# Kernel tuning notes

Hardware: AMD Instinct MI355X
Metric: run time of the kernel (lower is better)

The kernel has to match this reference:

```python
import jax, jax.numpy as jnp
import numpy as np

N_NODES = 50000
N_EDGES = 1600000
IN_DIM = 1024
HID = 128
N_GRAPHS = 64


def setup_inputs() -> dict:
    key = jax.random.key(0)
    ks = jax.random.split(key, 8)
    x = jax.random.normal(ks[0], (N_NODES, IN_DIM), dtype=jnp.float32)
    edge_index = jax.random.randint(ks[1], (2, N_EDGES), 0, N_NODES, dtype=jnp.int32)
    batch = jnp.sort(jax.random.randint(ks[2], (N_NODES,), 0, N_GRAPHS, dtype=jnp.int32))
    # GATConv parameters (single head, concat irrelevant for 1 head)
    glorot = 1.0 / np.sqrt(IN_DIM)
    W = jax.random.uniform(ks[3], (IN_DIM, HID), minval=-glorot, maxval=glorot, dtype=jnp.float32)
    ga = 1.0 / np.sqrt(HID)
    att_src = jax.random.uniform(ks[4], (HID,), minval=-ga, maxval=ga, dtype=jnp.float32)
    att_dst = jax.random.uniform(ks[5], (HID,), minval=-ga, maxval=ga, dtype=jnp.float32)
    bias = jnp.zeros((HID,), dtype=jnp.float32)
    return {"x": x, "W": W, "att_src": att_src, "att_dst": att_dst, "bias": bias,
            "edge_index": edge_index, "batch": batch, "num_graphs": N_GRAPHS}


def reference(x, W, att_src, att_dst, bias, edge_index, batch, num_graphs):
    N = x.shape[0]
    h = x @ W                               # [N, HID]
    # add self-loops (GATConv default add_self_loops=True)
    loops = jnp.arange(N, dtype=edge_index.dtype)
    src = jnp.concatenate([edge_index[0], loops])   # [E+N]
    dst = jnp.concatenate([edge_index[1], loops])
    a_src = h @ att_src                     # [N]
    a_dst = h @ att_dst                     # [N]
    e = jax.nn.leaky_relu(a_src[src] + a_dst[dst], negative_slope=0.2)  # [E+N]
    # scatter-softmax over incoming edges of each destination node
    m = jax.ops.segment_max(e, dst, num_segments=N)
    p = jnp.exp(e - m[dst])
    denom = jax.ops.segment_sum(p, dst, num_segments=N)
    alpha = p / denom[dst]                  # [E+N]
    # attention-weighted aggregation
    out = jax.ops.segment_sum(alpha[:, None] * h[src], dst, num_segments=N)  # [N, HID]
    out = jax.nn.relu(out + bias)
    # global max pool over graphs in the batch
    return jax.ops.segment_max(out, batch, num_segments=num_graphs)          # [G, HID]
```

## Files before the change

### kernel.cpp

```cpp
#include <hip/hip_runtime.h>
#include <hip/hip_bf16.h>

#define N_NODES 50000
#define N_EDGES 1600000
#define IN_DIM 1024
#define HID 128
#define AGG_WAVES 6144

typedef __bf16 bf16x8 __attribute__((ext_vector_type(8)));
typedef float f32x4 __attribute__((ext_vector_type(4)));
typedef __bf16 bf16x4 __attribute__((ext_vector_type(4)));

__device__ __forceinline__ float2 bf2f(unsigned u) {
    return make_float2(__uint_as_float(u << 16), __uint_as_float(u & 0xffff0000u));
}
__device__ __forceinline__ float lrelu(float v) { return v > 0.f ? v : 0.2f * v; }

__global__ void init_kernel(int* __restrict__ deg, float* __restrict__ out, int out_n) {
    int i = blockIdx.x * 256 + threadIdx.x;
    if (i < N_NODES) deg[i] = 0;
    if (i < out_n) out[i] = 0.0f;
}

__global__ void wtrans_kernel(const float* __restrict__ W, __bf16* __restrict__ wt) {
    int i = blockIdx.x * 256 + threadIdx.x;
    int n = i >> 10, k = i & 1023;
    wt[i] = (__bf16)W[(size_t)k * HID + n];
}

__global__ __launch_bounds__(256) void gemm_kernel(const float* __restrict__ x,
                                                   const __bf16* __restrict__ wt,
                                                   __bf16* __restrict__ h2,
                                                   const float* __restrict__ att_s,
                                                   const float* __restrict__ att_d,
                                                   float* __restrict__ o_as,
                                                   float* __restrict__ o_ad) {
    __shared__ __bf16 xa[128][40];
    __shared__ __bf16 wb[128][40];
    const int t = threadIdx.x;
    const int m0 = blockIdx.x * 128;
    const int wid = t >> 6, lane = t & 63;
    const int lm = lane & 15, q8 = (lane >> 4) * 8;
    const int rw0 = wid * 32;

    f32x4 acc[2][8] = {};
    for (int k0 = 0; k0 < IN_DIM; k0 += 32) {
#pragma unroll
        for (int l = 0; l < 4; ++l) {
            int f = t + l * 256;
            int row = f >> 3, kq = f & 7;
            int gr = m0 + row;
            float4 v = make_float4(0.f, 0.f, 0.f, 0.f);
            if (gr < N_NODES)
                v = *(const float4*)(x + (size_t)gr * IN_DIM + k0 + kq * 4);
            bf16x4 b; b[0] = (__bf16)v.x; b[1] = (__bf16)v.y; b[2] = (__bf16)v.z; b[3] = (__bf16)v.w;
            *(bf16x4*)&xa[row][kq * 4] = b;
        }
#pragma unroll
        for (int l = 0; l < 4; ++l) {
            int f = t + l * 256;
            int n = f >> 3, c = f & 7;
            *(uint2*)&wb[n][c * 4] = *(const uint2*)(wt + (size_t)n * IN_DIM + k0 + c * 4);
        }
        __syncthreads();
        bf16x8 af0 = *(const bf16x8*)&xa[rw0 + lm][q8];
        bf16x8 af1 = *(const bf16x8*)&xa[rw0 + 16 + lm][q8];
#pragma unroll
        for (int ct = 0; ct < 8; ++ct) {
            bf16x8 bfr = *(const bf16x8*)&wb[ct * 16 + lm][q8];
            acc[0][ct] = __builtin_amdgcn_mfma_f32_16x16x32_bf16(af0, bfr, acc[0][ct], 0, 0, 0);
            acc[1][ct] = __builtin_amdgcn_mfma_f32_16x16x32_bf16(af1, bfr, acc[1][ct], 0, 0, 0);
        }
        __syncthreads();
    }
    const int quad = lane >> 4;
    float attsf[8], attdf[8];
#pragma unroll
    for (int ct = 0; ct < 8; ++ct) {
        attsf[ct] = att_s[ct * 16 + lm];
        attdf[ct] = att_d[ct * 16 + lm];
    }
#pragma unroll
    for (int rt = 0; rt < 2; ++rt) {
#pragma unroll
        for (int reg = 0; reg < 4; ++reg) {
            int row = m0 + rw0 + rt * 16 + quad * 4 + reg;
            float ps = 0.f, pd = 0.f;
#pragma unroll
            for (int ct = 0; ct < 8; ++ct) {
                float v = acc[rt][ct][reg];
                ps = fmaf(v, attsf[ct], ps);
                pd = fmaf(v, attdf[ct], pd);
            }
#pragma unroll
            for (int o = 8; o; o >>= 1) {
                ps += __shfl_xor(ps, o);
                pd += __shfl_xor(pd, o);
            }
            if (row < N_NODES) {
                if (lm == 0) { o_as[row] = ps; o_ad[row] = pd; }
#pragma unroll
                for (int ct = 0; ct < 8; ++ct)
                    h2[(size_t)row * HID + ct * 16 + lm] = (__bf16)acc[rt][ct][reg];
            }
        }
    }
}

__global__ void hist_kernel(const int* __restrict__ ei, int* __restrict__ deg) {
    int e = blockIdx.x * 256 + threadIdx.x;
    if (e < N_EDGES) atomicAdd(&deg[ei[N_EDGES + e]], 1);
}

__global__ void scan1_kernel(const int* __restrict__ deg, int* __restrict__ bsum) {
    int b = blockIdx.x, t = threadIdx.x;
    int base = b * 1024 + t * 4;
    int s = 0;
#pragma unroll
    for (int j = 0; j < 4; ++j) {
        int idx = base + j;
        if (idx < N_NODES) s += deg[idx];
    }
    for (int o = 32; o; o >>= 1) s += __shfl_xor(s, o);
    __shared__ int wsum[4];
    int lane = t & 63, w = t >> 6;
    if (lane == 0) wsum[w] = s;
    __syncthreads();
    if (t == 0) bsum[b] = wsum[0] + wsum[1] + wsum[2] + wsum[3];
}

__global__ void scan2_kernel(const int* __restrict__ bsum, int* __restrict__ boff,
                             int* __restrict__ rowstart, int nb) {
    if (threadIdx.x == 0 && blockIdx.x == 0) {
        int run = 0;
        for (int i = 0; i < nb; ++i) { boff[i] = run; run += bsum[i]; }
        rowstart[N_NODES] = run;
    }
}

__global__ void scan3_kernel(int* __restrict__ deg, const int* __restrict__ boff,
                             int* __restrict__ rowstart) {
    int b = blockIdx.x, t = threadIdx.x;
    int base = b * 1024 + t * 4;
    int v[4]; int s = 0;
#pragma unroll
    for (int j = 0; j < 4; ++j) {
        int idx = base + j;
        v[j] = (idx < N_NODES) ? deg[idx] : 0;
        s += v[j];
    }
    int lane = t & 63, w = t >> 6;
    int inc = s;
    for (int o = 1; o < 64; o <<= 1) {
        int u = __shfl_up(inc, o);
        if (lane >= o) inc += u;
    }
    __shared__ int wt[4];
    if (lane == 63) wt[w] = inc;
    __syncthreads();
    int woff = 0;
    for (int i = 0; i < w; ++i) woff += wt[i];
    int run = woff + inc - s + boff[b];
#pragma unroll
    for (int j = 0; j < 4; ++j) {
        int idx = base + j;
        if (idx < N_NODES) {
            rowstart[idx] = run;
            run += v[j];
            deg[idx] = 0;
        }
    }
}

__global__ void scatter_kernel(const int* __restrict__ ei, const int* __restrict__ rowstart,
                               int* __restrict__ cursor, uint2* __restrict__ csrp,
                               const float* __restrict__ a_src) {
    int e = blockIdx.x * 256 + threadIdx.x;
    if (e >= N_EDGES) return;
    int s = ei[e], d = ei[N_EDGES + e];
    int pos = atomicAdd(&cursor[d], 1);
    uint2 v; v.x = (unsigned)s; v.y = __float_as_uint(a_src[s]);
    csrp[rowstart[d] + pos] = v;
}

__global__ __launch_bounds__(256, 6) void aggregate_kernel(
    const unsigned* __restrict__ h2u, const float* __restrict__ a_src,
    const float* __restrict__ a_dst, const int* __restrict__ rowstart,
    const uint2* __restrict__ csrp, const float* __restrict__ bias,
    const int* __restrict__ batch, float* __restrict__ out) {
    const int wid = threadIdx.x >> 6, lane = threadIdx.x & 63;
    const int w = blockIdx.x * 4 + wid;
    const int q = N_NODES / AGG_WAVES;
    const int r = N_NODES - q * AGG_WAVES;
    int n0 = w * q + (w < r ? w : r);
    int n1 = n0 + q + (w < r ? 1 : 0);
    const float b0 = bias[2 * lane], b1 = bias[2 * lane + 1];

    int gcur = -1;
    float m0 = 0.f, m1 = 0.f;
    for (int n = n0; n < n1; ++n) {
        int rs = rowstart[n], re = rowstart[n + 1];
        float adn = a_dst[n];
        float pself = __expf(lrelu(a_src[n] + adn));
        float2 hv = bf2f(h2u[(size_t)n * 64 + lane]);
        float denom = pself;
        float2 acc = make_float2(pself * hv.x, pself * hv.y);
        for (int base = rs; base < re; base += 64) {
            int cnt = re - base; if (cnt > 64) cnt = 64;
            uint2 sp = make_uint2(0u, 0u);
            bool valid = (base + lane < re);
            if (valid) sp = csrp[base + lane];
            float pe = valid ? __expf(lrelu(__uint_as_float(sp.y) + adn)) : 0.f;
            float ds = pe;
            for (int o = 32; o; o >>= 1) ds += __shfl_xor(ds, o);
            denom += ds;
            for (int e = 0; e < cnt; e += 16) {
                unsigned uu[16]; float pp[16];
#pragma unroll
                for (int i = 0; i < 16; ++i) {
                    unsigned src = (unsigned)__shfl((int)sp.x, e + i);
                    pp[i] = __shfl(pe, e + i);
                    uu[i] = h2u[(size_t)src * 64 + lane];
                }
#pragma unroll
                for (int i = 0; i < 16; ++i) {
                    float2 g = bf2f(uu[i]);
                    acc.x = fmaf(pp[i], g.x, acc.x);
                    acc.y = fmaf(pp[i], g.y, acc.y);
                }
            }
        }
        float inv = 1.0f / denom;
        float o0 = fmaxf(acc.x * inv + b0, 0.0f);
        float o1 = fmaxf(acc.y * inv + b1, 0.0f);
        int g = batch[n];
        if (g != gcur) {
            if (gcur >= 0) {
                unsigned* outp = (unsigned*)(out + (size_t)gcur * HID);
                atomicMax(&outp[2 * lane], __float_as_uint(m0));
                atomicMax(&outp[2 * lane + 1], __float_as_uint(m1));
            }
            gcur = g; m0 = o0; m1 = o1;
        } else {
            m0 = fmaxf(m0, o0); m1 = fmaxf(m1, o1);
        }
    }
    if (gcur >= 0) {
        unsigned* outp = (unsigned*)(out + (size_t)gcur * HID);
        atomicMax(&outp[2 * lane], __float_as_uint(m0));
        atomicMax(&outp[2 * lane + 1], __float_as_uint(m1));
    }
}

extern "C" void kernel_launch(void* const* d_in, const int* in_sizes, int n_in,
                              void* d_out, int out_size, void* d_ws, size_t ws_size,
                              hipStream_t stream) {
    const float* x     = (const float*)d_in[0];
    const float* W     = (const float*)d_in[1];
    const float* att_s = (const float*)d_in[2];
    const float* att_d = (const float*)d_in[3];
    const float* bias  = (const float*)d_in[4];
    const int*   ei    = (const int*)d_in[5];
    const int*   batch = (const int*)d_in[6];
    float*       out   = (float*)d_out;

    char* ws = (char*)d_ws;
    size_t off = 0;
    auto alloc = [&](size_t bytes) -> void* {
        void* p = ws + off;
        off += (bytes + 255) & ~(size_t)255;
        return p;
    };
    const int NB = (N_NODES + 1023) / 1024;
    __bf16* h2       = (__bf16*)alloc((size_t)N_NODES * HID * 2);
    __bf16* wt       = (__bf16*)alloc((size_t)HID * IN_DIM * 2);
    float*  a_src    = (float*)alloc((size_t)N_NODES * 4);
    float*  a_dst    = (float*)alloc((size_t)N_NODES * 4);
    int*    deg      = (int*)alloc((size_t)N_NODES * 4);
    int*    rowstart = (int*)alloc((size_t)(N_NODES + 1) * 4);
    int*    bsum     = (int*)alloc((size_t)NB * 4);
    int*    boff     = (int*)alloc((size_t)NB * 4);
    uint2*  csrp     = (uint2*)alloc((size_t)N_EDGES * 8);
    (void)ws_size; (void)in_sizes; (void)n_in;

    int init_n = (N_NODES > out_size ? N_NODES : out_size);
    hipLaunchKernelGGL(init_kernel, dim3((init_n + 255) / 256), dim3(256), 0, stream,
                       deg, out, out_size);
    hipLaunchKernelGGL(wtrans_kernel, dim3((HID * IN_DIM) / 256), dim3(256), 0, stream,
                       W, wt);
    hipLaunchKernelGGL(gemm_kernel, dim3((N_NODES + 127) / 128), dim3(256), 0, stream,
                       x, wt, h2, att_s, att_d, a_src, a_dst);
    hipLaunchKernelGGL(hist_kernel, dim3((N_EDGES + 255) / 256), dim3(256), 0, stream,
                       ei, deg);
    hipLaunchKernelGGL(scan1_kernel, dim3(NB), dim3(256), 0, stream, deg, bsum);
    hipLaunchKernelGGL(scan2_kernel, dim3(1), dim3(64), 0, stream, bsum, boff, rowstart, NB);
    hipLaunchKernelGGL(scan3_kernel, dim3(NB), dim3(256), 0, stream, deg, boff, rowstart);
    hipLaunchKernelGGL(scatter_kernel, dim3((N_EDGES + 255) / 256), dim3(256), 0, stream,
                       ei, rowstart, deg, csrp, a_src);
    hipLaunchKernelGGL(aggregate_kernel, dim3(AGG_WAVES / 4), dim3(256), 0, stream,
                       (const unsigned*)h2, a_src, a_dst, rowstart, csrp, bias, batch, out);
}
```

Baseline: 570.8 us.

## Halve GEMM tile rows, prefetch next K-slice into registers, merge prep kernels

The GEMM block tile shrinks from 128 to 64 rows, which doubles the grid size. The global loads for the next K-slice are issued into registers before the MFMAs on the current slice, overlapping memory latency with compute. The init and weight-transpose kernels are merged into one launch. The cost is that each W tile is reloaded by twice as many blocks, and each iteration now has an extra barrier.

Measured after the change: 540.1 us. 1.06x faster.

```diff
diff --git a/kernel.cpp b/kernel.cpp
--- a/kernel.cpp
+++ b/kernel.cpp
@@ -16,16 +16,15 @@
 }
 __device__ __forceinline__ float lrelu(float v) { return v > 0.f ? v : 0.2f * v; }
 
-__global__ void init_kernel(int* __restrict__ deg, float* __restrict__ out, int out_n) {
+__global__ void prep_kernel(const float* __restrict__ W, __bf16* __restrict__ wt,
+                            int* __restrict__ deg, float* __restrict__ out, int out_n) {
     int i = blockIdx.x * 256 + threadIdx.x;
     if (i < N_NODES) deg[i] = 0;
     if (i < out_n) out[i] = 0.0f;
-}
-
-__global__ void wtrans_kernel(const float* __restrict__ W, __bf16* __restrict__ wt) {
-    int i = blockIdx.x * 256 + threadIdx.x;
-    int n = i >> 10, k = i & 1023;
-    wt[i] = (__bf16)W[(size_t)k * HID + n];
+    if (i < HID * IN_DIM) {
+        int n = i >> 10, k = i & 1023;
+        wt[i] = (__bf16)W[(size_t)k * HID + n];
+    }
 }
 
 __global__ __launch_bounds__(256) void gemm_kernel(const float* __restrict__ x,
@@ -35,43 +34,73 @@
                                                    const float* __restrict__ att_d,
                                                    float* __restrict__ o_as,
                                                    float* __restrict__ o_ad) {
-    __shared__ __bf16 xa[128][40];
+    __shared__ __bf16 xa[64][40];
     __shared__ __bf16 wb[128][40];
     const int t = threadIdx.x;
-    const int m0 = blockIdx.x * 128;
+    const int m0 = blockIdx.x * 64;
     const int wid = t >> 6, lane = t & 63;
     const int lm = lane & 15, q8 = (lane >> 4) * 8;
-    const int rw0 = wid * 32;
-
-    f32x4 acc[2][8] = {};
-    for (int k0 = 0; k0 < IN_DIM; k0 += 32) {
-#pragma unroll
-        for (int l = 0; l < 4; ++l) {
+    const int rw0 = wid * 16;
+
+    const int xrow = t >> 2, xkq = (t & 3);
+    const int wn = t >> 1, wc2 = (t & 1);
+
+    float4 xs_reg[2];
+    uint2  ws_reg[4];
+
+    auto stage_regs = [&](int k0) {
+#pragma unroll
+        for (int l = 0; l < 2; ++l) {
             int f = t + l * 256;
             int row = f >> 3, kq = f & 7;
             int gr = m0 + row;
             float4 v = make_float4(0.f, 0.f, 0.f, 0.f);
             if (gr < N_NODES)
                 v = *(const float4*)(x + (size_t)gr * IN_DIM + k0 + kq * 4);
-            bf16x4 b; b[0] = (__bf16)v.x; b[1] = (__bf16)v.y; b[2] = (__bf16)v.z; b[3] = (__bf16)v.w;
-            *(bf16x4*)&xa[row][kq * 4] = b;
+            xs_reg[l] = v;
         }
 #pragma unroll
         for (int l = 0; l < 4; ++l) {
             int f = t + l * 256;
             int n = f >> 3, c = f & 7;
-            *(uint2*)&wb[n][c * 4] = *(const uint2*)(wt + (size_t)n * IN_DIM + k0 + c * 4);
-        }
-        __syncthreads();
-        bf16x8 af0 = *(const bf16x8*)&xa[rw0 + lm][q8];
-        bf16x8 af1 = *(const bf16x8*)&xa[rw0 + 16 + lm][q8];
+            ws_reg[l] = *(const uint2*)(wt + (size_t)n * IN_DIM + k0 + c * 4);
+        }
+    };
+    auto regs_to_lds = [&]() {
+#pragma unroll
+        for (int l = 0; l < 2; ++l) {
+            int f = t + l * 256;
+            int row = f >> 3, kq = f & 7;
+            bf16x4 b;
+            b[0] = (__bf16)xs_reg[l].x; b[1] = (__bf16)xs_reg[l].y;
+            b[2] = (__bf16)xs_reg[l].z; b[3] = (__bf16)xs_reg[l].w;
+            *(bf16x4*)&xa[row][kq * 4] = b;
+        }
+#pragma unroll
+        for (int l = 0; l < 4; ++l) {
+            int f = t + l * 256;
+            int n = f >> 3, c = f & 7;
+            *(uint2*)&wb[n][c * 4] = ws_reg[l];
+        }
+    };
+
+    f32x4 acc[8] = {};
+    stage_regs(0);
+    regs_to_lds();
+    __syncthreads();
+    for (int it = 0; it < 32; ++it) {
+        if (it + 1 < 32) stage_regs((it + 1) * 32);
+        bf16x8 af = *(const bf16x8*)&xa[rw0 + lm][q8];
 #pragma unroll
         for (int ct = 0; ct < 8; ++ct) {
             bf16x8 bfr = *(const bf16x8*)&wb[ct * 16 + lm][q8];
-            acc[0][ct] = __builtin_amdgcn_mfma_f32_16x16x32_bf16(af0, bfr, acc[0][ct], 0, 0, 0);
-            acc[1][ct] = __builtin_amdgcn_mfma_f32_16x16x32_bf16(af1, bfr, acc[1][ct], 0, 0, 0);
-        }
-        __syncthreads();
+            acc[ct] = __builtin_amdgcn_mfma_f32_16x16x32_bf16(af, bfr, acc[ct], 0, 0, 0);
+        }
+        if (it + 1 < 32) {
+            __syncthreads();
+            regs_to_lds();
+            __syncthreads();
+        }
     }
     const int quad = lane >> 4;
     float attsf[8], attdf[8];
@@ -81,30 +110,28 @@
         attdf[ct] = att_d[ct * 16 + lm];
     }
 #pragma unroll
-    for (int rt = 0; rt < 2; ++rt) {
-#pragma unroll
-        for (int reg = 0; reg < 4; ++reg) {
-            int row = m0 + rw0 + rt * 16 + quad * 4 + reg;
-            float ps = 0.f, pd = 0.f;
-#pragma unroll
-            for (int ct = 0; ct < 8; ++ct) {
-                float v = acc[rt][ct][reg];
-                ps = fmaf(v, attsf[ct], ps);
-                pd = fmaf(v, attdf[ct], pd);
-            }
-#pragma unroll
-            for (int o = 8; o; o >>= 1) {
-                ps += __shfl_xor(ps, o);
-                pd += __shfl_xor(pd, o);
-            }
-            if (row < N_NODES) {
-                if (lm == 0) { o_as[row] = ps; o_ad[row] = pd; }
-#pragma unroll
-                for (int ct = 0; ct < 8; ++ct)
-                    h2[(size_t)row * HID + ct * 16 + lm] = (__bf16)acc[rt][ct][reg];
-            }
-        }
-    }
+    for (int reg = 0; reg < 4; ++reg) {
+        int row = m0 + rw0 + quad * 4 + reg;
+        float ps = 0.f, pd = 0.f;
+#pragma unroll
+        for (int ct = 0; ct < 8; ++ct) {
+            float v = acc[ct][reg];
+            ps = fmaf(v, attsf[ct], ps);
+            pd = fmaf(v, attdf[ct], pd);
+        }
+#pragma unroll
+        for (int o = 8; o; o >>= 1) {
+            ps += __shfl_xor(ps, o);
+            pd += __shfl_xor(pd, o);
+        }
+        if (row < N_NODES) {
+            if (lm == 0) { o_as[row] = ps; o_ad[row] = pd; }
+#pragma unroll
+            for (int ct = 0; ct < 8; ++ct)
+                h2[(size_t)row * HID + ct * 16 + lm] = (__bf16)acc[ct][reg];
+        }
+    }
+    (void)xrow; (void)xkq; (void)wn; (void)wc2;
 }
 
 __global__ void hist_kernel(const int* __restrict__ ei, int* __restrict__ deg) {
@@ -283,12 +310,9 @@
     uint2*  csrp     = (uint2*)alloc((size_t)N_EDGES * 8);
     (void)ws_size; (void)in_sizes; (void)n_in;
 
-    int init_n = (N_NODES > out_size ? N_NODES : out_size);
-    hipLaunchKernelGGL(init_kernel, dim3((init_n + 255) / 256), dim3(256), 0, stream,
-                       deg, out, out_size);
-    hipLaunchKernelGGL(wtrans_kernel, dim3((HID * IN_DIM) / 256), dim3(256), 0, stream,
-                       W, wt);
-    hipLaunchKernelGGL(gemm_kernel, dim3((N_NODES + 127) / 128), dim3(256), 0, stream,
+    hipLaunchKernelGGL(prep_kernel, dim3(512), dim3(256), 0, stream,
+                       W, wt, deg, out, out_size);
+    hipLaunchKernelGGL(gemm_kernel, dim3((N_NODES + 63) / 64), dim3(256), 0, stream,
                        x, wt, h2, att_s, att_d, a_src, a_dst);
     hipLaunchKernelGGL(hist_kernel, dim3((N_EDGES + 255) / 256), dim3(256), 0, stream,
                        ei, deg);
```
